# Performance work log

Hardware: AMD Instinct MI355X
Metric: run time of the kernel (lower is better)

The kernel has to match this reference:

```python
import jax, jax.numpy as jnp
import numpy as np

B, N, C = 2, 2048, 1024
H = 16
R = 4
MLP = 4096
LORA_SCALE = 1.0 / R  # lora_alpha=1, r=4
EPS = 1e-5


def _ln(x, g, b):
    m = jnp.mean(x, axis=-1, keepdims=True)
    v = jnp.mean(jnp.square(x - m), axis=-1, keepdims=True)
    return (x - m) * jax.lax.rsqrt(v + EPS) * g + b


def setup_inputs() -> dict:
    key = jax.random.key(0)
    ks = jax.random.split(key, 16)
    s = lambda k, shape, fan: jax.random.normal(k, shape, jnp.float32) * (1.0 / np.sqrt(fan))
    return {
        "x": jax.random.normal(ks[0], (B, N, C), jnp.float32),
        "pos": jax.random.normal(ks[1], (B, N, C), jnp.float32),
        "Wqkv": s(ks[2], (3 * C, C), C),
        "b_qkv": jnp.zeros((3 * C,), jnp.float32),
        "lora_A": s(ks[3], (2 * R, C), C),          # rows 0:R -> q, R:2R -> v
        "lora_B": s(ks[4], (2 * C, R), R) * 0.1,     # rows 0:C -> q, C:2C -> v
        "Wproj": s(ks[5], (C, C), C),
        "b_proj": jnp.zeros((C,), jnp.float32),
        "ln1_g": jnp.ones((C,), jnp.float32),
        "ln1_b": jnp.zeros((C,), jnp.float32),
        "ln2_g": jnp.ones((C,), jnp.float32),
        "ln2_b": jnp.zeros((C,), jnp.float32),
        "W1": s(ks[6], (MLP, C), C),
        "b1": jnp.zeros((MLP,), jnp.float32),
        "W2": s(ks[7], (C, MLP), MLP),
        "b2": jnp.zeros((C,), jnp.float32),
        "idx": 0,
    }


def reference(x, pos, Wqkv, b_qkv, lora_A, lora_B, Wproj, b_proj,
              ln1_g, ln1_b, ln2_g, ln2_b, W1, b1, W2, b2, idx):
    # (dropout layers are identity in eval mode)
    x = x + pos

    # --- attention block: Residual(PreNormDrop(SelfAttention)) ---
    h = _ln(x, ln1_g, ln1_b)                              # [B,N,C]
    qkv = h @ Wqkv.T + b_qkv                              # [B,N,3C]
    # LoRA MergedLinear: low-rank update on q and v thirds only
    after_A = h @ lora_A.T                                # [B,N,2R]
    dq = after_A[..., :R] @ lora_B[:C].T * LORA_SCALE     # [B,N,C]
    dv = after_A[..., R:] @ lora_B[C:].T * LORA_SCALE     # [B,N,C]
    qkv = qkv.at[..., :C].add(dq).at[..., 2 * C:].add(dv)

    Dh = C // H
    q, k, v = [t.reshape(B, N, H, Dh).transpose(0, 2, 1, 3)
               for t in jnp.split(qkv, 3, axis=-1)]       # each [B,H,N,Dh]
    scale = Dh ** -0.5
    attn = jnp.einsum('bhid,bhjd->bhij', q, k) * scale    # [B,H,N,N]
    attn = jax.nn.softmax(attn, axis=-1)
    o = jnp.einsum('bhij,bhjd->bhid', attn, v)            # [B,H,N,Dh]
    o = o.transpose(0, 2, 1, 3).reshape(B, N, C)
    o = o @ Wproj.T + b_proj
    x = x + o

    # --- FFN block: Residual(PreNorm(FeedForward)) ---
    h2 = _ln(x, ln2_g, ln2_b)
    h2 = jax.nn.gelu(h2 @ W1.T + b1, approximate=False)
    h2 = h2 @ W2.T + b2
    return x + h2
```

## Files before the change

kernel.cpp:

```cpp
#include <hip/hip_runtime.h>
#include <hip/hip_bf16.h>
#include <math.h>

typedef __hip_bfloat16 bf16;
typedef __attribute__((ext_vector_type(4))) float f32x4;
typedef __attribute__((ext_vector_type(16))) float f32x16;
typedef __attribute__((ext_vector_type(8))) short s16x8;

__device__ __forceinline__ void async_cp16(void* lds, const void* g) {
    __builtin_amdgcn_global_load_lds((const __attribute__((address_space(1))) void*)g,
                                     (__attribute__((address_space(3))) void*)lds, 16, 0, 0);
}

__device__ __forceinline__ float gelu_fast(float x) {
    float y = 1.5957691216f * (x + 0.044715f * x * x * x);
    float t = __expf(y);
    float th = 1.0f - 2.0f / (t + 1.0f);
    return 0.5f * x * (1.0f + th);
}

__global__ __launch_bounds__(256)
void cvt_all(const float* __restrict__ w0, const float* __restrict__ w1,
             const float* __restrict__ w2, const float* __restrict__ w3,
             bf16* __restrict__ o0, bf16* __restrict__ o1,
             bf16* __restrict__ o2, bf16* __restrict__ o3) {
    int i = blockIdx.x * 256 + threadIdx.x;
    const float* src; bf16* dst; int j = i;
    if (j < 786432)            { src = w0; dst = o0; }
    else if (j < 1048576)      { j -= 786432;  src = w1; dst = o1; }
    else if (j < 2097152)      { j -= 1048576; src = w2; dst = o2; }
    else                       { j -= 2097152; src = w3; dst = o3; }
    float4 v = ((const float4*)src)[j];
    union { bf16 o[4]; uint2 u; } pk;
    pk.o[0] = __float2bfloat16(v.x); pk.o[1] = __float2bfloat16(v.y);
    pk.o[2] = __float2bfloat16(v.z); pk.o[3] = __float2bfloat16(v.w);
    ((uint2*)dst)[j] = pk.u;
}

template <bool ADD>
__global__ __launch_bounds__(256)
void ln_kernel(const float* __restrict__ xin, const float* __restrict__ pos,
               const float* __restrict__ gam, const float* __restrict__ bet,
               float* __restrict__ x1, bf16* __restrict__ hout,
               const float* __restrict__ loraA, float* __restrict__ afterA) {
    const int row = blockIdx.x, tid = threadIdx.x;
    const size_t off = (size_t)row * 1024;
    float4 v = ((const float4*)(xin + off))[tid];
    if constexpr (ADD) {
        float4 p = ((const float4*)(pos + off))[tid];
        v.x += p.x; v.y += p.y; v.z += p.z; v.w += p.w;
        ((float4*)(x1 + off))[tid] = v;
    }
    float s  = v.x + v.y + v.z + v.w;
    float s2 = v.x*v.x + v.y*v.y + v.z*v.z + v.w*v.w;
#pragma unroll
    for (int o = 32; o >= 1; o >>= 1) { s += __shfl_xor(s, o); s2 += __shfl_xor(s2, o); }
    __shared__ float sS[4], sS2[4];
    int w = tid >> 6, lane = tid & 63;
    if (lane == 0) { sS[w] = s; sS2[w] = s2; }
    __syncthreads();
    float mean = (sS[0] + sS[1] + sS[2] + sS[3]) * (1.f / 1024.f);
    float e2   = (sS2[0] + sS2[1] + sS2[2] + sS2[3]) * (1.f / 1024.f);
    float rstd = rsqrtf(e2 - mean * mean + 1e-5f);
    float4 gv = ((const float4*)gam)[tid], bv = ((const float4*)bet)[tid];
    float h0 = (v.x - mean) * rstd * gv.x + bv.x;
    float h1 = (v.y - mean) * rstd * gv.y + bv.y;
    float h2 = (v.z - mean) * rstd * gv.z + bv.z;
    float h3 = (v.w - mean) * rstd * gv.w + bv.w;
    bf16* ho = hout + off + tid * 4;
    ho[0] = __float2bfloat16(h0);
    ho[1] = __float2bfloat16(h1);
    ho[2] = __float2bfloat16(h2);
    ho[3] = __float2bfloat16(h3);
    if constexpr (ADD) {
        float p[8];
#pragma unroll
        for (int r = 0; r < 8; r++) {
            float4 av = ((const float4*)(loraA + (size_t)r * 1024))[tid];
            p[r] = h0 * av.x + h1 * av.y + h2 * av.z + h3 * av.w;
        }
#pragma unroll
        for (int r = 0; r < 8; r++)
#pragma unroll
            for (int o = 32; o >= 1; o >>= 1) p[r] += __shfl_xor(p[r], o);
        __shared__ float red[4][8];
        if (lane == 0) {
#pragma unroll
            for (int r = 0; r < 8; r++) red[w][r] = p[r];
        }
        __syncthreads();
        if (tid < 8) afterA[(size_t)row * 8 + tid] = red[0][tid] + red[1][tid] + red[2][tid] + red[3][tid];
    }
}

template <int MODE>
__global__ __launch_bounds__(512, 2)
void gemm_bk64(const bf16* __restrict__ A, const bf16* __restrict__ B,
               const float* __restrict__ bias, bf16* __restrict__ outp,
               const float* __restrict__ afterA, const float* __restrict__ loraB,
               bf16* __restrict__ Qb, bf16* __restrict__ Kb, bf16* __restrict__ Vt,
               int M, int N, int K, int gx) {
    __shared__ bf16 As[2][256 * 64];
    __shared__ bf16 Bs[2][256 * 64];
    const int tid = threadIdx.x;
    const int lane = tid & 63, w = tid >> 6;
    const int grp = lane >> 4, c16 = lane & 15;
    const int wm = (w & 1) * 128, wn = (w >> 1) * 64;
    const int nwg = gridDim.x, bid = blockIdx.x;
    const int sw = (bid & 7) * (nwg >> 3) + (bid >> 3);
    const int bm = (sw / gx) * 256, bn = (sw % gx) * 256;

    f32x4 acc[8][4];
    const f32x4 zero = {0.f, 0.f, 0.f, 0.f};
#pragma unroll
    for (int mi = 0; mi < 8; mi++)
#pragma unroll
        for (int ni = 0; ni < 4; ni++) acc[mi][ni] = zero;

#define STAGE256(bufi, k0)                                                          \
    {                                                                               \
        const int buf_ = (bufi);                                                    \
        const int koff_ = (k0);                                                     \
        _Pragma("unroll") for (int t_ = 0; t_ < 4; t_++) {                          \
            int s_ = t_ * 512 + tid;                                                \
            int row_ = s_ >> 3, db_ = s_ & 7;                                       \
            int gb_ = (db_ ^ (row_ & 7)) << 3;                                      \
            async_cp16(&As[buf_][s_ * 8], A + (size_t)(bm + row_) * K + koff_ + gb_); \
            async_cp16(&Bs[buf_][s_ * 8], B + (size_t)(bn + row_) * K + koff_ + gb_); \
        }                                                                           \
    }

#define COMPUTE256(bufi)                                                            \
    {                                                                               \
        const int buf_ = (bufi);                                                    \
        _Pragma("unroll") for (int kc_ = 0; kc_ < 2; kc_++) {                       \
            s16x8 af_[8], bfv_[4];                                                  \
            _Pragma("unroll") for (int mi_ = 0; mi_ < 8; mi_++) {                   \
                int r_ = wm + mi_ * 16 + c16;                                       \
                af_[mi_] = *(const s16x8*)&As[buf_][r_ * 64 + ((((kc_ << 2) | grp) ^ (r_ & 7)) << 3)]; \
            }                                                                       \
            _Pragma("unroll") for (int ni_ = 0; ni_ < 4; ni_++) {                   \
                int r_ = wn + ni_ * 16 + c16;                                       \
                bfv_[ni_] = *(const s16x8*)&Bs[buf_][r_ * 64 + ((((kc_ << 2) | grp) ^ (r_ & 7)) << 3)]; \
            }                                                                       \
            _Pragma("unroll") for (int mi_ = 0; mi_ < 8; mi_++)                     \
                _Pragma("unroll") for (int ni_ = 0; ni_ < 4; ni_++)                 \
                    acc[mi_][ni_] = __builtin_amdgcn_mfma_f32_16x16x32_bf16(af_[mi_], bfv_[ni_], acc[mi_][ni_], 0, 0, 0); \
        }                                                                           \
    }

#define WAITV8 asm volatile("s_waitcnt vmcnt(8)" ::: "memory")
#define WAITV0 asm volatile("s_waitcnt vmcnt(0)" ::: "memory")

#define STEP256(BQ, TQ)                                                             \
    {                                                                               \
        const int tq_ = (TQ);                                                       \
        COMPUTE256(BQ);                                                             \
        __builtin_amdgcn_s_barrier();            \
        if (tq_ + 2 < nk) { STAGE256(BQ, (tq_ + 2) << 6); WAITV8; }                 \
        else { WAITV0; }                                \
        __builtin_amdgcn_s_barrier();             \
    }

    const int nk = K >> 6;
    STAGE256(0, 0);
    STAGE256(1, 64);
    WAITV8;
    __builtin_amdgcn_s_barrier();

    for (int t = 0; t < nk - 2; t += 2) {
        STEP256(0, t);
        STEP256(1, t + 1);
    }
    STEP256(0, nk - 2);
    COMPUTE256(1);

#undef STEP256
#undef WAITV8
#undef WAITV0
#undef STAGE256
#undef COMPUTE256

    if constexpr (MODE == 1) {
        const int role = bn >> 10;
        const int g_b  = bm >> 11;
        if (role == 2) {
            char* tp = (char*)&Bs[0][0];
            const int tokb = bm & 2047;
#pragma unroll
            for (int pass = 0; pass < 2; pass++) {
                if ((wm >> 7) == pass) {
#pragma unroll
                    for (int mi = 0; mi < 8; mi++) {
                        float4 aA4[4];
#pragma unroll
                        for (int q = 0; q < 4; q++) {
                            int grow = bm + wm + mi * 16 + grp * 4 + q;
                            aA4[q] = ((const float4*)afterA)[(size_t)grow * 2 + 1];
                        }
#pragma unroll
                        for (int ni = 0; ni < 4; ni++) {
                            int fl = wn + ni * 16 + c16;
                            int cr = (bn & 1023) + fl;
                            float bv = bias[bn + fl];
                            float4 bw = ((const float4*)loraB)[1024 + cr];
                            union { bf16 e[4]; uint2 u; } pk;
#pragma unroll
                            for (int q = 0; q < 4; q++) {
                                float dv = (aA4[q].x*bw.x + aA4[q].y*bw.y + aA4[q].z*bw.z + aA4[q].w*bw.w) * 0.25f;
                                pk.e[q] = __float2bfloat16(acc[mi][ni][q] + bv + dv);
                            }
                            int tl = mi * 16 + grp * 4;
                            int off = (fl * 256 + tl * 2) ^ ((fl & 7) << 3);
                            *(uint2*)(tp + off) = pk.u;
                        }
                    }
                }
                __syncthreads();
#pragma unroll
                for (int it = 0; it < 16; it++) {
                    int s = it * 512 + tid;
                    int fl = s >> 5, c4 = s & 31;
                    int off = (fl * 256 + c4 * 8) ^ ((fl & 7) << 3);
                    uint2 v = *(uint2*)(tp + off);
                    int cr = (bn & 1023) + fl;
                    int h = cr >> 6, d = cr & 63;
                    *(uint2*)&Vt[((size_t)(g_b * 16 + h) * 64 + d) * 2048 + tokb + pass * 128 + c4 * 4] = v;
                }
                if (pass == 0) __syncthreads();
            }
        } else if (role == 0) {
#pragma unroll
            for (int mi = 0; mi < 8; mi++) {
                float4 aA4[4];
#pragma unroll
                for (int q = 0; q < 4; q++) {
                    int grow = bm + wm + mi * 16 + grp * 4 + q;
                    aA4[q] = ((const float4*)afterA)[(size_t)grow * 2];
                }
#pragma unroll
                for (int ni = 0; ni < 4; ni++) {
                    int c  = bn + wn + ni * 16 + c16;
                    int cr = c & 1023;
                    int h  = cr >> 6, d = cr & 63;
                    float bv = bias[c];
                    float4 bw = ((const float4*)loraB)[cr];
#pragma unroll
                    for (int q = 0; q < 4; q++) {
                        int grow = bm + wm + mi * 16 + grp * 4 + q;
                        float dq = (aA4[q].x*bw.x + aA4[q].y*bw.y + aA4[q].z*bw.z + aA4[q].w*bw.w) * 0.25f;
                        float v = (acc[mi][ni][q] + bv + dq) * 0.18033688011f;
                        Qb[((size_t)(g_b * 16 + h) * 2048 + (grow & 2047)) * 64 + d] = __float2bfloat16(v);
                    }
                }
            }
        } else {
#pragma unroll
            for (int mi = 0; mi < 8; mi++)
#pragma unroll
                for (int ni = 0; ni < 4; ni++) {
                    int c  = bn + wn + ni * 16 + c16;
                    int cr = c & 1023;
                    int h  = cr >> 6, d = cr & 63;
                    float bv = bias[c];
#pragma unroll
                    for (int q = 0; q < 4; q++) {
                        int grow = bm + wm + mi * 16 + grp * 4 + q;
                        Kb[((size_t)(g_b * 16 + h) * 2048 + (grow & 2047)) * 64 + d] =
                            __float2bfloat16(acc[mi][ni][q] + bv);
                    }
                }
        }
    } else {
#pragma unroll
        for (int mi = 0; mi < 8; mi++)
#pragma unroll
            for (int ni = 0; ni < 4; ni++) {
                int r0 = bm + wm + mi * 16 + grp * 4;
                int c  = bn + wn + ni * 16 + c16;
                float bv = bias[c];
#pragma unroll
                for (int q = 0; q < 4; q++) {
                    size_t idx = (size_t)(r0 + q) * N + c;
                    float v = acc[mi][ni][q] + bv;
                    if constexpr (MODE == 2) v = gelu_fast(v);
                    outp[idx] = __float2bfloat16(v);
                }
            }
    }
}

__global__ __launch_bounds__(256)
void gemm_n64(const bf16* __restrict__ A, const bf16* __restrict__ B,
              const float* __restrict__ bias, const float* __restrict__ resid,
              float* __restrict__ outp, int M, int N, int K, int gx) {
    __shared__ bf16 As[3][128 * 64];
    __shared__ bf16 Bs[3][64 * 64];
    const int tid = threadIdx.x;
    const int lane = tid & 63, w = tid >> 6;
    const int grp = lane >> 4, c16 = lane & 15;
    const int wm = w * 32;
    const int nwg = gridDim.x, bid = blockIdx.x;
    const int sw = (bid & 7) * (nwg >> 3) + (bid >> 3);
    const int bm = (sw / gx) * 128, bn = (sw % gx) * 64;

    f32x4 acc[2][4];
    const f32x4 zero = {0.f, 0.f, 0.f, 0.f};
#pragma unroll
    for (int mi = 0; mi < 2; mi++)
#pragma unroll
        for (int ni = 0; ni < 4; ni++) acc[mi][ni] = zero;

#define STAGE64(bufi, k0)                                                           \
    {                                                                               \
        const int buf_ = (bufi);                                                    \
        const int koff_ = (k0);                                                     \
        _Pragma("unroll") for (int t_ = 0; t_ < 4; t_++) {                          \
            int s_ = t_ * 256 + tid;                                                \
            int row_ = s_ >> 3, db_ = s_ & 7;                                       \
            async_cp16(&As[buf_][s_ * 8], A + (size_t)(bm + row_) * K + koff_ + ((db_ ^ (row_ & 7)) << 3)); \
        }                                                                           \
        _Pragma("unroll") for (int t_ = 0; t_ < 2; t_++) {                          \
            int s_ = t_ * 256 + tid;                                                \
            int row_ = s_ >> 3, db_ = s_ & 7;                                       \
            async_cp16(&Bs[buf_][s_ * 8], B + (size_t)(bn + row_) * K + koff_ + ((db_ ^ (row_ & 7)) << 3)); \
        }                                                                           \
    }

#define COMPUTE64(bufi)                                                             \
    {                                                                               \
        const int buf_ = (bufi);                                                    \
        _Pragma("unroll") for (int kc_ = 0; kc_ < 2; kc_++) {                       \
            s16x8 af_[2], bfv_[4];                                                  \
            _Pragma("unroll") for (int mi_ = 0; mi_ < 2; mi_++) {                   \
                int r_ = wm + mi_ * 16 + c16;                                       \
                af_[mi_] = *(const s16x8*)&As[buf_][r_ * 64 + ((((kc_ << 2) | grp) ^ (r_ & 7)) << 3)]; \
            }                                                                       \
            _Pragma("unroll") for (int ni_ = 0; ni_ < 4; ni_++) {                   \
                int rb_ = ni_ * 16 + c16;                                           \
                bfv_[ni_] = *(const s16x8*)&Bs[buf_][rb_ * 64 + ((((kc_ << 2) | grp) ^ (rb_ & 7)) << 3)]; \
            }                                                                       \
            _Pragma("unroll") for (int mi_ = 0; mi_ < 2; mi_++)                     \
                _Pragma("unroll") for (int ni_ = 0; ni_ < 4; ni_++)                 \
                    acc[mi_][ni_] = __builtin_amdgcn_mfma_f32_16x16x32_bf16(af_[mi_], bfv_[ni_], acc[mi_][ni_], 0, 0, 0); \
        }                                                                           \
    }

#define WAITV12 asm volatile("s_waitcnt vmcnt(12)" ::: "memory")
#define WAITV6  asm volatile("s_waitcnt vmcnt(6)"  ::: "memory")
#define WAITV0  asm volatile("s_waitcnt vmcnt(0)"  ::: "memory")

#define STEP64(BQ, TQ)                                                              \
    {                                                                               \
        const int tq_ = (TQ);                                                       \
        COMPUTE64(BQ);                                                              \
        __builtin_amdgcn_s_barrier();            \
        if (tq_ + 3 < nk) { STAGE64(BQ, (tq_ + 3) << 6); WAITV12; }                 \
        else if (tq_ + 2 < nk) { WAITV6; }                                          \
        else { WAITV0; }                                \
        __builtin_amdgcn_s_barrier();             \
    }

    const int nk = K >> 6;
    STAGE64(0, 0);
    STAGE64(1, 64);
    STAGE64(2, 128);
    WAITV12;
    __builtin_amdgcn_s_barrier();

    for (int t = 0; t < nk - 1; t += 3) {
        STEP64(0, t);
        STEP64(1, t + 1);
        STEP64(2, t + 2);
    }
    COMPUTE64(0);

#undef STEP64
#undef WAITV12
#undef WAITV6
#undef WAITV0
#undef STAGE64
#undef COMPUTE64

#pragma unroll
    for (int mi = 0; mi < 2; mi++)
#pragma unroll
        for (int ni = 0; ni < 4; ni++) {
            int r0 = bm + wm + mi * 16 + grp * 4;
            int c  = bn + ni * 16 + c16;
            float bv = bias[c];
#pragma unroll
            for (int q = 0; q < 4; q++) {
                size_t idx = (size_t)(r0 + q) * N + c;
                outp[idx] = acc[mi][ni][q] + bv + resid[idx];
            }
        }
}

__global__ __launch_bounds__(256)
void attn_fused(const bf16* __restrict__ Qb, const bf16* __restrict__ Kb,
                const bf16* __restrict__ Vt, bf16* __restrict__ Og) {
    __shared__ bf16 Qs[128 * 64], Ks[2][64 * 64], Vs[2][64 * 64];
    const int tid = threadIdx.x;
    const int lane = tid & 63, w = tid >> 6;
    const int c32 = lane & 31, l5 = lane >> 5;
    const int bid = blockIdx.x;
    const int sw = (bid & 7) * 64 + (bid >> 3);
    const int bh = sw >> 4, b = bh >> 4, h = bh & 15;
    const int i0 = (sw & 15) * 128;
    const int rowperm = (c32 & 19) | (((c32 >> 3) & 1) << 2) | (((c32 >> 2) & 1) << 3);

    const size_t qbase = (size_t)(bh * 2048 + i0) * 64;
    const size_t kbase = (size_t)bh * 2048 * 64;
    const size_t vbase = (size_t)bh * 64 * 2048;

#define STAGEKV(bufi, jv)                                                           \
    {                                                                               \
        const int buf_ = (bufi);                                                    \
        const int joff_ = (jv);                                                     \
        _Pragma("unroll") for (int t_ = 0; t_ < 2; t_++) {                          \
            int s_ = t_ * 256 + tid;                                                \
            int row_ = s_ >> 3, db_ = s_ & 7;                                       \
            int gb_ = (db_ ^ (row_ & 7)) << 3;                                      \
            async_cp16(&Ks[buf_][s_ * 8], Kb + kbase + (size_t)(joff_ + row_) * 64 + gb_); \
            async_cp16(&Vs[buf_][s_ * 8], Vt + vbase + (size_t)row_ * 2048 + joff_ + gb_); \
        }                                                                           \
    }

#pragma unroll
    for (int t = 0; t < 4; t++) {
        int s = t * 256 + tid;
        int row = s >> 3, db = s & 7;
        async_cp16(&Qs[s * 8], Qb + qbase + row * 64 + ((db ^ (row & 7)) << 3));
    }
    STAGEKV(0, 0);
    __syncthreads();

    s16x8 qf[4];
    {
        int rq = w * 32 + c32;
#pragma unroll
        for (int kc = 0; kc < 4; kc++) {
            int db = 2 * kc + l5;
            qf[kc] = *(const s16x8*)&Qs[rq * 64 + ((db ^ (rq & 7)) << 3)];
        }
    }

    f32x16 Oq[2];
#pragma unroll
    for (int dq = 0; dq < 2; dq++)
#pragma unroll
        for (int r = 0; r < 16; r++) Oq[dq][r] = 0.f;
    float l_lane = 0.f;

#define ATILE(BUF, JN)                                                              \
    {                                                                               \
        const int jn_ = (JN);                                                       \
        if (jn_ < 32) { STAGEKV((BUF) ^ 1, jn_ << 6); }                             \
        f32x16 Sq[2];                                                               \
        __builtin_amdgcn_s_setprio(1);                                              \
        _Pragma("unroll") for (int jq_ = 0; jq_ < 2; jq_++) {                       \
            _Pragma("unroll") for (int r_ = 0; r_ < 16; r_++) Sq[jq_][r_] = 0.f;    \
            int rk_ = jq_ * 32 + rowperm;                                           \
            _Pragma("unroll") for (int kc_ = 0; kc_ < 4; kc_++) {                   \
                int db_ = 2 * kc_ + l5;                                             \
                s16x8 af_ = *(const s16x8*)&Ks[BUF][rk_ * 64 + ((db_ ^ (rk_ & 7)) << 3)]; \
                Sq[jq_] = __builtin_amdgcn_mfma_f32_32x32x16_bf16(af_, qf[kc_], Sq[jq_], 0, 0, 0); \
            }                                                                       \
        }                                                                           \
        __builtin_amdgcn_s_setprio(0);                                              \
        s16x8 pf_[4];                                                               \
        _Pragma("unroll") for (int kc_ = 0; kc_ < 4; kc_++) {                       \
            union { s16x8 v; unsigned u4[4]; } u_;                                  \
            _Pragma("unroll") for (int pr_ = 0; pr_ < 4; pr_++) {                   \
                float a_ = Sq[kc_ >> 1][8 * (kc_ & 1) + 2 * pr_];                   \
                float b_ = Sq[kc_ >> 1][8 * (kc_ & 1) + 2 * pr_ + 1];               \
                float pa_, pb_;                                                     \
                asm("v_exp_f32 %0, %1" : "=v"(pa_) : "v"(a_));                      \
                asm("v_exp_f32 %0, %1" : "=v"(pb_) : "v"(b_));                      \
                l_lane += pa_; l_lane += pb_;                                       \
                unsigned pk_;                                                       \
                asm("v_cvt_pk_bf16_f32 %0, %1, %2" : "=v"(pk_) : "v"(pa_), "v"(pb_)); \
                u_.u4[pr_] = pk_;                                                   \
            }                                                                       \
            pf_[kc_] = u_.v;                                                        \
        }                                                                           \
        __builtin_amdgcn_s_setprio(1);                                              \
        _Pragma("unroll") for (int dq_ = 0; dq_ < 2; dq_++) {                       \
            int rd_ = dq_ * 32 + c32;                                               \
            _Pragma("unroll") for (int kc_ = 0; kc_ < 4; kc_++) {                   \
                int jb_ = 2 * kc_ + l5;                                             \
                s16x8 af_ = *(const s16x8*)&Vs[BUF][rd_ * 64 + ((jb_ ^ (rd_ & 7)) << 3)]; \
                Oq[dq_] = __builtin_amdgcn_mfma_f32_32x32x16_bf16(af_, pf_[kc_], Oq[dq_], 0, 0, 0); \
            }                                                                       \
        }                                                                           \
        __builtin_amdgcn_s_setprio(0);                                              \
        __syncthreads();                                                            \
    }

    for (int jt = 0; jt < 32; jt += 2) {
        ATILE(0, jt + 1);
        ATILE(1, jt + 2);
    }
#undef ATILE
#undef STAGEKV

    float l = l_lane + __shfl_xor(l_lane, 32);
    float inv = 1.0f / fmaxf(l, 1e-35f);
    int i = i0 + w * 32 + c32;
    size_t obase = (size_t)(b * 2048 + i) * 1024 + h * 64;
#pragma unroll
    for (int dq = 0; dq < 2; dq++)
#pragma unroll
        for (int rg = 0; rg < 4; rg++) {
            union { bf16 e[4]; uint2 u; } pk;
#pragma unroll
            for (int c = 0; c < 4; c++)
                pk.e[c] = __float2bfloat16(Oq[dq][rg * 4 + c] * inv);
            int d0 = dq * 32 + l5 * 4 + rg * 8;
            *(uint2*)&Og[obase + d0] = pk.u;
        }
}

extern "C" void kernel_launch(void* const* d_in, const int* in_sizes, int n_in,
                              void* d_out, int out_size, void* d_ws, size_t ws_size,
                              hipStream_t stream) {
    const float* x     = (const float*)d_in[0];
    const float* pos   = (const float*)d_in[1];
    const float* Wqkv  = (const float*)d_in[2];
    const float* bqkv  = (const float*)d_in[3];
    const float* loraA = (const float*)d_in[4];
    const float* loraB = (const float*)d_in[5];
    const float* Wproj = (const float*)d_in[6];
    const float* bproj = (const float*)d_in[7];
    const float* ln1g  = (const float*)d_in[8];
    const float* ln1b  = (const float*)d_in[9];
    const float* ln2g  = (const float*)d_in[10];
    const float* ln2b  = (const float*)d_in[11];
    const float* W1    = (const float*)d_in[12];
    const float* b1    = (const float*)d_in[13];
    const float* W2    = (const float*)d_in[14];
    const float* b2    = (const float*)d_in[15];

    char* ws = (char*)d_ws;
    float* x1     = (float*)(ws + 0);
    bf16*  hbuf   = (bf16*) (ws + 16777216);
    bf16*  gbuf   = (bf16*) (ws + 50331648);
    float* afterA = (float*)(ws + 83886080);
    bf16*  Qb     = (bf16*) (ws + 84017152);
    bf16*  Kb     = (bf16*) (ws + 92405760);
    bf16*  Vt     = (bf16*) (ws + 100794368);
    bf16*  Obf    = (bf16*) (ws + 109182976);
    bf16*  Wqkvb  = (bf16*) (ws + 117571584);
    bf16*  Wprojb = (bf16*) (ws + 123863040);
    bf16*  W1b    = (bf16*) (ws + 125960192);
    bf16*  W2b    = (bf16*) (ws + 134348800);

    cvt_all<<<12288, 256, 0, stream>>>(Wqkv, Wproj, W1, W2, Wqkvb, Wprojb, W1b, W2b);

    ln_kernel<true><<<4096, 256, 0, stream>>>(x, pos, ln1g, ln1b, x1, hbuf, loraA, afterA);

    gemm_bk64<1><<<192, 512, 0, stream>>>(hbuf, Wqkvb, bqkv, nullptr,
                                          afterA, loraB, Qb, Kb, Vt,
                                          4096, 3072, 1024, 12);

    attn_fused<<<512, 256, 0, stream>>>(Qb, Kb, Vt, Obf);

    gemm_n64<<<512, 256, 0, stream>>>(Obf, Wprojb, bproj, x1, x1, 4096, 1024, 1024, 16);

    ln_kernel<false><<<4096, 256, 0, stream>>>(x1, nullptr, ln2g, ln2b, nullptr, hbuf, nullptr, nullptr);

    gemm_bk64<2><<<256, 512, 0, stream>>>(hbuf, W1b, b1, gbuf,
                                          nullptr, nullptr, nullptr, nullptr, nullptr,
                                          4096, 4096, 1024, 16);

    gemm_n64<<<512, 256, 0, stream>>>(gbuf, W2b, b2, x1, (float*)d_out, 4096, 1024, 4096, 16);

    (void)in_sizes; (void)n_in; (void)out_size; (void)ws_size;
}
```

Baseline: 360.2 us.

## Split-K the W2 down-projection GEMM with 128x128 tiles and partial-sum add

Replaces the W2 GEMM (M=4096, N=1024, K=4096) with a 2-way split-K kernel that uses 128x128 tiles, giving 512 workgroups. The first K half adds bias and residual into the output, the second writes raw partials to a workspace buffer, and a separate elementwise kernel then adds the two. The aim is better CU utilization and more reuse per tile on a long-K GEMM. In exchange it writes and reads an extra 16MB fp32 partial buffer and adds one kernel launch.

```diff
diff --git a/kernel.cpp b/kernel.cpp
--- a/kernel.cpp
+++ b/kernel.cpp
@@ -398,6 +398,127 @@
 }
 
 __global__ __launch_bounds__(256)
+void gemm_w2sk(const bf16* __restrict__ A, const bf16* __restrict__ B,
+               const float* __restrict__ bias, const float* __restrict__ resid,
+               float* __restrict__ outp, float* __restrict__ part1,
+               int M, int N, int K, int gx) {
+    __shared__ bf16 As[2][128 * 64];
+    __shared__ bf16 Bs[2][128 * 64];
+    const int tid = threadIdx.x;
+    const int lane = tid & 63, w = tid >> 6;
+    const int grp = lane >> 4, c16 = lane & 15;
+    const int wm = (w & 1) * 64, wn = (w >> 1) * 64;
+    const int nwg = gridDim.x, bid = blockIdx.x;
+    const int sw = (bid & 7) * (nwg >> 3) + (bid >> 3);
+    const int ks = sw >> 8;
+    const int id2 = sw & 255;
+    const int bm = (id2 / gx) * 128, bn = (id2 % gx) * 128;
+    const int kbase = ks * (K >> 1);
+
+    f32x4 acc[4][4];
+    const f32x4 zero = {0.f, 0.f, 0.f, 0.f};
+#pragma unroll
+    for (int mi = 0; mi < 4; mi++)
+#pragma unroll
+        for (int ni = 0; ni < 4; ni++) acc[mi][ni] = zero;
+
+#define STAGEW2(bufi, k0)                                                           \
+    {                                                                               \
+        const int buf_ = (bufi);                                                    \
+        const int koff_ = kbase + (k0);                                             \
+        _Pragma("unroll") for (int t_ = 0; t_ < 4; t_++) {                          \
+            int s_ = t_ * 256 + tid;                                                \
+            int row_ = s_ >> 3, db_ = s_ & 7;                                       \
+            int gb_ = (db_ ^ (row_ & 7)) << 3;                                      \
+            async_cp16(&As[buf_][s_ * 8], A + (size_t)(bm + row_) * K + koff_ + gb_); \
+            async_cp16(&Bs[buf_][s_ * 8], B + (size_t)(bn + row_) * K + koff_ + gb_); \
+        }                                                                           \
+    }
+
+#define COMPUTEW2(bufi)                                                             \
+    {                                                                               \
+        const int buf_ = (bufi);                                                    \
+        _Pragma("unroll") for (int kc_ = 0; kc_ < 2; kc_++) {                       \
+            s16x8 af_[4], bfv_[4];                                                  \
+            _Pragma("unroll") for (int mi_ = 0; mi_ < 4; mi_++) {                   \
+                int r_ = wm + mi_ * 16 + c16;                                       \
+                af_[mi_] = *(const s16x8*)&As[buf_][r_ * 64 + ((((kc_ << 2) | grp) ^ (r_ & 7)) << 3)]; \
+            }                                                                       \
+            _Pragma("unroll") for (int ni_ = 0; ni_ < 4; ni_++) {                   \
+                int r_ = wn + ni_ * 16 + c16;                                       \
+                bfv_[ni_] = *(const s16x8*)&Bs[buf_][r_ * 64 + ((((kc_ << 2) | grp) ^ (r_ & 7)) << 3)]; \
+            }                                                                       \
+            _Pragma("unroll") for (int mi_ = 0; mi_ < 4; mi_++)                     \
+                _Pragma("unroll") for (int ni_ = 0; ni_ < 4; ni_++)                 \
+                    acc[mi_][ni_] = __builtin_amdgcn_mfma_f32_16x16x32_bf16(af_[mi_], bfv_[ni_], acc[mi_][ni_], 0, 0, 0); \
+        }                                                                           \
+    }
+
+#define WAITV8 asm volatile("s_waitcnt vmcnt(8)" ::: "memory")
+#define WAITV0 asm volatile("s_waitcnt vmcnt(0)" ::: "memory")
+
+#define STEPW2(BQ, TQ)                                                              \
+    {                                                                               \
+        const int tq_ = (TQ);                                                       \
+        COMPUTEW2(BQ);                                                              \
+        __builtin_amdgcn_s_barrier();                                               \
+        if (tq_ + 2 < nk) { STAGEW2(BQ, (tq_ + 2) << 6); WAITV8; }                  \
+        else { WAITV0; }                                                            \
+        __builtin_amdgcn_s_barrier();                                               \
+    }
+
+    const int nk = K >> 7;
+    STAGEW2(0, 0);
+    STAGEW2(1, 64);
+    WAITV8;
+    __builtin_amdgcn_s_barrier();
+
+    for (int t = 0; t < nk - 2; t += 2) {
+        STEPW2(0, t);
+        STEPW2(1, t + 1);
+    }
+    STEPW2(0, nk - 2);
+    COMPUTEW2(1);
+
+#undef STEPW2
+#undef WAITV8
+#undef WAITV0
+#undef STAGEW2
+#undef COMPUTEW2
+
+#pragma unroll
+    for (int mi = 0; mi < 4; mi++)
+#pragma unroll
+        for (int ni = 0; ni < 4; ni++) {
+            int r0 = bm + wm + mi * 16 + grp * 4;
+            int c  = bn + wn + ni * 16 + c16;
+            if (ks == 0) {
+                float bv = bias[c];
+#pragma unroll
+                for (int q = 0; q < 4; q++) {
+                    size_t idx = (size_t)(r0 + q) * N + c;
+                    outp[idx] = acc[mi][ni][q] + bv + resid[idx];
+                }
+            } else {
+#pragma unroll
+                for (int q = 0; q < 4; q++) {
+                    size_t idx = (size_t)(r0 + q) * N + c;
+                    part1[idx] = acc[mi][ni][q];
+                }
+            }
+        }
+}
+
+__global__ __launch_bounds__(256)
+void add_part(float* __restrict__ outp, const float* __restrict__ p1) {
+    int i = blockIdx.x * 256 + threadIdx.x;
+    float4 a = ((float4*)outp)[i];
+    float4 b = ((const float4*)p1)[i];
+    a.x += b.x; a.y += b.y; a.z += b.z; a.w += b.w;
+    ((float4*)outp)[i] = a;
+}
+
+__global__ __launch_bounds__(256)
 void attn_fused(const bf16* __restrict__ Qb, const bf16* __restrict__ Kb,
                 const bf16* __restrict__ Vt, bf16* __restrict__ Og) {
     __shared__ bf16 Qs[128 * 64], Ks[2][64 * 64], Vs[2][64 * 64];
@@ -545,6 +666,7 @@
     char* ws = (char*)d_ws;
     float* x1     = (float*)(ws + 0);
     bf16*  hbuf   = (bf16*) (ws + 16777216);
+    float* part1  = (float*)(ws + 25165824);
     bf16*  gbuf   = (bf16*) (ws + 50331648);
     float* afterA = (float*)(ws + 83886080);
     bf16*  Qb     = (bf16*) (ws + 84017152);
@@ -574,7 +696,9 @@
                                           nullptr, nullptr, nullptr, nullptr, nullptr,
                                           4096, 4096, 1024, 16);
 
-    gemm_n64<<<512, 256, 0, stream>>>(gbuf, W2b, b2, x1, (float*)d_out, 4096, 1024, 4096, 16);
+    gemm_w2sk<<<512, 256, 0, stream>>>(gbuf, W2b, b2, x1, (float*)d_out, part1,
+                                       4096, 1024, 4096, 8);
+    add_part<<<4096, 256, 0, stream>>>((float*)d_out, part1);
 
     (void)in_sizes; (void)n_in; (void)out_size; (void)ws_size;
 }
```

Measured after the change: 355.2 us. Within noise of the previous version (-1.4%).
